# Optimization experiments

Hardware: AMD Instinct MI355X
Metric: run time of the kernel (lower is better)

The kernel has to match this reference:

```python
import jax, jax.numpy as jnp
import numpy as np

V, C, H, L, FC, OUT, WS = 512, 256, 4, 6, 1024, 192, 4
HD = C // H
B, T = 8, 1024


def setup_inputs() -> dict:
    key = jax.random.key(0)
    ks = jax.random.split(key, 24)
    d = {}
    d['emb'] = jax.random.normal(ks[0], (V, C), jnp.float32) * C ** -0.5
    d['Wq'] = jax.random.normal(ks[1], (L, C, C), jnp.float32) * 0.02
    d['Wk'] = jax.random.normal(ks[2], (L, C, C), jnp.float32) * 0.02
    d['Wv'] = jax.random.normal(ks[3], (L, C, C), jnp.float32) * 0.02
    d['Wo'] = jax.random.normal(ks[4], (L, C, C), jnp.float32) * 0.02
    d['bq'] = jnp.zeros((L, C), jnp.float32)
    d['bk'] = jnp.zeros((L, C), jnp.float32)
    d['bv'] = jnp.zeros((L, C), jnp.float32)
    d['bo'] = jnp.zeros((L, C), jnp.float32)
    d['rel_k'] = jax.random.normal(ks[5], (L, 2 * WS + 1, HD), jnp.float32) * HD ** -0.5
    d['rel_v'] = jax.random.normal(ks[6], (L, 2 * WS + 1, HD), jnp.float32) * HD ** -0.5
    d['ln1_g'] = jnp.ones((L, C), jnp.float32)
    d['ln1_b'] = jnp.zeros((L, C), jnp.float32)
    d['ln2_g'] = jnp.ones((L, C), jnp.float32)
    d['ln2_b'] = jnp.zeros((L, C), jnp.float32)
    d['ffn_w1'] = jax.random.normal(ks[7], (L, C, FC), jnp.float32) * 0.02
    d['ffn_b1'] = jnp.zeros((L, FC), jnp.float32)
    d['ffn_w2'] = jax.random.normal(ks[8], (L, FC, C), jnp.float32) * 0.02
    d['ffn_b2'] = jnp.zeros((L, C), jnp.float32)
    d['proj_w'] = jax.random.normal(ks[9], (2 * OUT, C), jnp.float32) * 0.02
    d['proj_b'] = jnp.zeros((2 * OUT,), jnp.float32)
    d['tokens'] = jax.random.randint(ks[10], (B, T), 0, V)
    d['x_lengths'] = jax.random.randint(ks[11], (B,), T // 2, T + 1)
    return d


def _rel_to_abs(x):
    # x: [B,H,L,2L-1] -> [B,H,L,L]
    b, h, l, _ = x.shape
    x = jnp.pad(x, ((0, 0), (0, 0), (0, 0), (0, 1)))
    x = x.reshape(b, h, l * 2 * l)
    x = jnp.pad(x, ((0, 0), (0, 0), (0, l - 1)))
    x = x.reshape(b, h, l + 1, 2 * l - 1)
    return x[:, :, :l, l - 1:]


def _abs_to_rel(x):
    # x: [B,H,L,L] -> [B,H,L,2L-1]
    b, h, l, _ = x.shape
    x = jnp.pad(x, ((0, 0), (0, 0), (0, 0), (0, l - 1)))
    x = x.reshape(b, h, l * (2 * l - 1))
    x = jnp.pad(x, ((0, 0), (0, 0), (l, 0)))
    x = x.reshape(b, h, l, 2 * l)
    return x[:, :, :, 1:]


def _layernorm(x, g, b):
    m = jnp.mean(x, -1, keepdims=True)
    v = jnp.var(x, -1, keepdims=True)
    return (x - m) * jax.lax.rsqrt(v + 1e-5) * g + b


def _pad_rel(emb, t):
    # [2*WS+1, HD] -> [2t-1, HD] (t > WS+1 here)
    p = t - (WS + 1)
    return jnp.pad(emb, ((p, p), (0, 0)))


def _forward(emb, Wq, Wk, Wv, Wo, bq, bk, bv, bo, rel_k, rel_v, ln1_g, ln1_b,
             ln2_g, ln2_b, ffn_w1, ffn_b1, ffn_w2, ffn_b2, proj_w, proj_b,
             tokens, x_lengths):
    b, t = tokens.shape
    x = emb[tokens] * jnp.sqrt(jnp.float32(C))          # [B,T,C]
    mask = (jnp.arange(t)[None, :] < x_lengths[:, None]).astype(x.dtype)  # [B,T]
    attn_mask = mask[:, None, None, :] * mask[:, None, :, None]           # [B,1,T,T]

    for i in range(L):
        q = (x @ Wq[i] + bq[i]).reshape(b, t, H, HD).transpose(0, 2, 1, 3)
        k = (x @ Wk[i] + bk[i]).reshape(b, t, H, HD).transpose(0, 2, 1, 3)
        v = (x @ Wv[i] + bv[i]).reshape(b, t, H, HD).transpose(0, 2, 1, 3)
        q = q * HD ** -0.5
        scores = jnp.einsum('bhqd,bhkd->bhqk', q, k)
        rk = _pad_rel(rel_k[i], t)                      # [2T-1,HD]
        scores = scores + _rel_to_abs(jnp.einsum('bhqd,md->bhqm', q, rk))
        scores = jnp.where(attn_mask > 0, scores, -1e4)
        p = jax.nn.softmax(scores, axis=-1)             # [B,H,T,T]
        o = jnp.einsum('bhqk,bhkd->bhqd', p, v)
        rv = _pad_rel(rel_v[i], t)
        o = o + jnp.einsum('bhqm,md->bhqd', _abs_to_rel(p), rv)
        o = o.transpose(0, 2, 1, 3).reshape(b, t, C) @ Wo[i] + bo[i]
        x = _layernorm(x + o, ln1_g[i], ln1_b[i])
        f = jax.nn.relu(x @ ffn_w1[i] + ffn_b1[i]) @ ffn_w2[i] + ffn_b2[i]
        x = _layernorm(x + f, ln2_g[i], ln2_b[i])
        x = x * mask[:, :, None]

    x_bct = x.transpose(0, 2, 1)                        # [B,C,T]
    stats = (jnp.einsum('oc,bct->bot', proj_w, x_bct) + proj_b[None, :, None])
    stats = stats * mask[:, None, :]
    m, logs = stats[:, :OUT], stats[:, OUT:]
    return x_bct, m, logs, mask[:, None, :]


def reference(emb, Wq, Wk, Wv, Wo, bq, bk, bv, bo, rel_k, rel_v, ln1_g, ln1_b,
              ln2_g, ln2_b, ffn_w1, ffn_b1, ffn_w2, ffn_b2, proj_w, proj_b,
              tokens, x_lengths):
    return _forward(emb, Wq, Wk, Wv, Wo, bq, bk, bv, bo, rel_k, rel_v, ln1_g,
                    ln1_b, ln2_g, ln2_b, ffn_w1, ffn_b1, ffn_w2, ffn_b2,
                    proj_w, proj_b, tokens, x_lengths)
```

## Files before the change

### kernel.cpp

```cpp
#include <hip/hip_runtime.h>

typedef unsigned short u16;
typedef __attribute__((ext_vector_type(8))) short bf16x8;
typedef __attribute__((ext_vector_type(4))) float f32x4;

#define CC   256
#define HH   4
#define HD   64
#define LL   6
#define FCD  1024
#define OUTD 192
#define WSZ  4
#define BB   8
#define TT   1024
#define BT   8192

#define OFF_XBCT 0
#define OFF_M    2097152
#define OFF_LOGS 3670016
#define OFF_MASK 5242880

#define WT_Q   0
#define WT_K   65536
#define WT_V   131072
#define WT_O   196608
#define WT_W1  262144
#define WT_W2  524288
#define WT_LAYER 786432
#define WT_TOTAL (6 * WT_LAYER)

__device__ __forceinline__ float bf2f(u16 u) {
  union { unsigned int i; float f; } v; v.i = ((unsigned int)u) << 16; return v.f;
}
__device__ __forceinline__ u16 f2bf(float f) {
  union { float f; unsigned int i; } v; v.f = f;
  unsigned int x = v.i;
  return (u16)((x + 0x7fffu + ((x >> 16) & 1u)) >> 16);
}
__device__ __forceinline__ void ldv4(const float* p, float* o) {
  float4 v = *reinterpret_cast<const float4*>(p);
  o[0] = v.x; o[1] = v.y; o[2] = v.z; o[3] = v.w;
}
__device__ __forceinline__ float ld_e(const float* p) { return *p; }
__device__ __forceinline__ float ld_e(const u16* p)   { return bf2f(*p); }
__device__ __forceinline__ void st_e(float* p, float v) { *p = v; }
__device__ __forceinline__ void st_e(u16* p, float v)   { *p = f2bf(v); }

__device__ __forceinline__ void gload16(const u16* g, u16* l) {
  __builtin_amdgcn_global_load_lds(
      (const __attribute__((address_space(1))) unsigned int*)g,
      (__attribute__((address_space(3))) unsigned int*)l, 16, 0, 0);
}

__device__ __forceinline__ void stage8(const float* p, u16* d) {
  float4 a = *reinterpret_cast<const float4*>(p);
  float4 b = *reinterpret_cast<const float4*>(p + 4);
  d[0] = f2bf(a.x); d[1] = f2bf(a.y); d[2] = f2bf(a.z); d[3] = f2bf(a.w);
  d[4] = f2bf(b.x); d[5] = f2bf(b.y); d[6] = f2bf(b.z); d[7] = f2bf(b.w);
}
__device__ __forceinline__ void stage8(const u16* p, u16* d) {
  ushort4 a = *reinterpret_cast<const ushort4*>(p);
  ushort4 b = *reinterpret_cast<const ushort4*>(p + 4);
  d[0] = a.x; d[1] = a.y; d[2] = a.z; d[3] = a.w;
  d[4] = b.x; d[5] = b.y; d[6] = b.z; d[7] = b.w;
}

__global__ __launch_bounds__(256) void tc_k(
    const float* __restrict__ W, u16* __restrict__ WT,
    int K, int N, int dstStride)
{
  __shared__ float tl[32][33];
  const int tid = threadIdx.x;
  const int lx = tid & 31;
  const int ly = tid >> 5;
  const int n0 = blockIdx.x << 5;
  const int k0 = blockIdx.y << 5;
  const int z  = blockIdx.z;
  const float* Ws = W + (size_t)z * K * N;
  u16* WTd = WT + (size_t)z * dstStride;
#pragma unroll
  for (int r = 0; r < 4; ++r)
    tl[ly + r * 8][lx] = Ws[(size_t)(k0 + ly + r * 8) * N + (n0 + lx)];
  __syncthreads();
#pragma unroll
  for (int r = 0; r < 4; ++r)
    WTd[(size_t)(n0 + ly + r * 8) * K + (k0 + lx)] = f2bf(tl[lx][ly + r * 8]);
}

__global__ __launch_bounds__(256) void embed_k(
    const float* __restrict__ emb, const int* __restrict__ tokens,
    float* __restrict__ X, u16* __restrict__ Xb)
{
  const int i = blockIdx.x * 256 + threadIdx.x;
  const int bt = i >> 6;
  const int c  = (i & 63) << 2;
  float4 e = *reinterpret_cast<const float4*>(emb + (size_t)tokens[bt] * CC + c);
  e.x *= 16.0f; e.y *= 16.0f; e.z *= 16.0f; e.w *= 16.0f;
  *reinterpret_cast<float4*>(X + (size_t)i * 4) = e;
  if (Xb)
    *reinterpret_cast<ushort4*>(Xb + (size_t)i * 4) =
        make_ushort4(f2bf(e.x), f2bf(e.y), f2bf(e.z), f2bf(e.w));
}

template <typename CT>
__global__ __launch_bounds__(256) void gemm_t_k(
    const u16* __restrict__ A, int lda, const u16* __restrict__ B, int ldb,
    const float* __restrict__ bias, CT* __restrict__ C, int ldc,
    int K, float ps, int relu, int accum)
{
  __shared__ __align__(16) u16 As[64 * 64];
  __shared__ __align__(16) u16 Bs[64 * 64];
  const int tid  = threadIdx.x;
  const int lane = tid & 63;
  const int wv   = tid >> 6;
  const int bm = blockIdx.y * 64;
  const int bn = blockIdx.x * 64;
  const int l15 = lane & 15;
  const int lq  = lane >> 4;
  const int sb0 = wv << 10;
  const int sb1 = sb0 + 512;
  const int r0  = (wv << 4) + (lane >> 3);
  const int r1  = r0 + 8;
  const int sc  = ((lane & 7) ^ (lane >> 3)) << 3;
  const int asw = (l15 & 7) << 3;

  f32x4 acc[4];
#pragma unroll
  for (int nt = 0; nt < 4; ++nt) acc[nt] = (f32x4){0.0f, 0.0f, 0.0f, 0.0f};

  for (int k0 = 0; k0 < K; k0 += 64) {
    gload16(A + (size_t)(bm + r0) * lda + (k0 + sc), As + sb0);
    gload16(A + (size_t)(bm + r1) * lda + (k0 + sc), As + sb1);
    gload16(B + (size_t)(bn + r0) * ldb + (k0 + sc), Bs + sb0);
    gload16(B + (size_t)(bn + r1) * ldb + (k0 + sc), Bs + sb1);
    __syncthreads();
#pragma unroll
    for (int s = 0; s < 2; ++s) {
      const int cbase = (s << 5) | (lq << 3);
      const bf16x8 af = *reinterpret_cast<const bf16x8*>(
          As + (((wv << 4) + l15) << 6) + (cbase ^ asw));
#pragma unroll
      for (int nt = 0; nt < 4; ++nt) {
        const bf16x8 bf = *reinterpret_cast<const bf16x8*>(
            Bs + (((nt << 4) + l15) << 6) + (cbase ^ asw));
        acc[nt] = __builtin_amdgcn_mfma_f32_16x16x32_bf16(af, bf, acc[nt], 0, 0, 0);
      }
    }
    __syncthreads();
  }

#pragma unroll
  for (int nt = 0; nt < 4; ++nt) {
#pragma unroll
    for (int r = 0; r < 4; ++r) {
      const int row = bm + (wv << 4) + (lq << 2) + r;
      const int col = bn + (nt << 4) + l15;
      float vv = acc[nt][r];
      if (bias) vv += bias[col];
      vv *= ps;
      if (relu) vv = fmaxf(vv, 0.0f);
      const size_t ci = (size_t)row * ldc + col;
      if (accum) vv += ld_e(C + ci);
      st_e(C + ci, vv);
    }
  }
}

__global__ __launch_bounds__(256) void gemm_qkv_k(
    const u16* __restrict__ Xb, const u16* __restrict__ WTl,
    const float* __restrict__ bq, const float* __restrict__ bk,
    const float* __restrict__ bv,
    u16* __restrict__ Qb, u16* __restrict__ Kb, u16* __restrict__ Vb)
{
  __shared__ __align__(16) u16 pool[2 * 64 * 64];
  u16* As = pool;
  u16* Bs = pool + 4096;
  const int tid  = threadIdx.x;
  const int lane = tid & 63;
  const int wv   = tid >> 6;
  const int bx = blockIdx.x;
  const int bm = blockIdx.y * 64;
  const int mi = bx >> 2;
  const int bnl = (bx & 3) << 6;
  const int bng = bx << 6;
  const int l15 = lane & 15;
  const int lq  = lane >> 4;
  const int sb0 = wv << 10;
  const int sb1 = sb0 + 512;
  const int r0  = (wv << 4) + (lane >> 3);
  const int r1  = r0 + 8;
  const int sc  = ((lane & 7) ^ (lane >> 3)) << 3;
  const int asw = (l15 & 7) << 3;

  const float* bias = (mi == 0) ? bq : (mi == 1) ? bk : bv;
  const float ps = (mi == 0) ? 0.125f : 1.0f;

  f32x4 acc[4];
#pragma unroll
  for (int nt = 0; nt < 4; ++nt) acc[nt] = (f32x4){0.0f, 0.0f, 0.0f, 0.0f};

  for (int k0 = 0; k0 < CC; k0 += 64) {
    gload16(Xb  + (size_t)(bm + r0) * CC + (k0 + sc), As + sb0);
    gload16(Xb  + (size_t)(bm + r1) * CC + (k0 + sc), As + sb1);
    gload16(WTl + (size_t)(bng + r0) * CC + (k0 + sc), Bs + sb0);
    gload16(WTl + (size_t)(bng + r1) * CC + (k0 + sc), Bs + sb1);
    __syncthreads();
#pragma unroll
    for (int s = 0; s < 2; ++s) {
      const int cbase = (s << 5) | (lq << 3);
      const bf16x8 af = *reinterpret_cast<const bf16x8*>(
          As + (((wv << 4) + l15) << 6) + (cbase ^ asw));
#pragma unroll
      for (int nt = 0; nt < 4; ++nt) {
        const bf16x8 bf = *reinterpret_cast<const bf16x8*>(
            Bs + (((nt << 4) + l15) << 6) + (cbase ^ asw));
        acc[nt] = __builtin_amdgcn_mfma_f32_16x16x32_bf16(af, bf, acc[nt], 0, 0, 0);
      }
    }
    __syncthreads();
  }

  if (mi != 2) {
    u16* Cp = (mi == 0) ? Qb : Kb;
#pragma unroll
    for (int nt = 0; nt < 4; ++nt) {
#pragma unroll
      for (int r = 0; r < 4; ++r) {
        const int row = bm + (wv << 4) + (lq << 2) + r;
        const int col = bnl + (nt << 4) + l15;
        Cp[(size_t)row * CC + col] = f2bf((acc[nt][r] + bias[col]) * ps);
      }
    }
  } else {
    u16* Ts = pool;
#pragma unroll
    for (int nt = 0; nt < 4; ++nt) {
#pragma unroll
      for (int r = 0; r < 4; ++r) {
        const int tl = (wv << 4) + (lq << 2) + r;
        const int dl = (nt << 4) + l15;
        Ts[dl * 72 + tl] = f2bf(acc[nt][r] + bias[bnl + dl]);
      }
    }
    __syncthreads();
    const int dl = tid >> 2;
    const size_t rowbase =
        ((size_t)((bm >> 10) * 256 + bnl + dl) << 10) + (bm & (TT - 1));
#pragma unroll
    for (int j = 0; j < 4; ++j) {
      const int c4 = ((tid & 3) << 2) + (j << 4);
      *reinterpret_cast<ushort4*>(Vb + rowbase + c4) =
          *reinterpret_cast<const ushort4*>(Ts + dl * 72 + c4);
    }
  }
}

__global__ __launch_bounds__(256) void gemm_ln_k(
    const u16* __restrict__ A, int lda, const u16* __restrict__ B, int ldb,
    const float* __restrict__ bias,
    float* __restrict__ X, u16* __restrict__ Xb,
    const float* __restrict__ g, const float* __restrict__ be,
    const int* __restrict__ xlen, int am, int K)
{
  __shared__ __align__(16) u16 As[16 * 64];
  __shared__ __align__(16) u16 Bs[256 * 64];
  __shared__ float part[16][4];
  __shared__ float part2[16][4];
  const int tid  = threadIdx.x;
  const int lane = tid & 63;
  const int wv   = tid >> 6;
  const int bm   = blockIdx.x << 4;
  const int l15  = lane & 15;
  const int lq   = lane >> 4;
  const int sc   = ((lane & 7) ^ (lane >> 3)) << 3;
  const int asw  = (l15 & 7) << 3;

  f32x4 acc[4];
#pragma unroll
  for (int nt = 0; nt < 4; ++nt) acc[nt] = (f32x4){0.0f, 0.0f, 0.0f, 0.0f};

  for (int k0 = 0; k0 < K; k0 += 64) {
    if (wv < 2)
      gload16(A + (size_t)(bm + (wv << 3) + (lane >> 3)) * lda + (k0 + sc),
              As + (wv << 9));
#pragma unroll
    for (int j = 0; j < 8; ++j)
      gload16(B + (size_t)((wv << 6) + (j << 3) + (lane >> 3)) * ldb + (k0 + sc),
              Bs + (wv << 12) + (j << 9));
    __syncthreads();
#pragma unroll
    for (int s = 0; s < 2; ++s) {
      const int cbase = (s << 5) | (lq << 3);
      const bf16x8 af = *reinterpret_cast<const bf16x8*>(
          As + (l15 << 6) + (cbase ^ asw));
#pragma unroll
      for (int nt = 0; nt < 4; ++nt) {
        const bf16x8 bf = *reinterpret_cast<const bf16x8*>(
            Bs + (((wv << 6) + (nt << 4) + l15) << 6) + (cbase ^ asw));
        acc[nt] = __builtin_amdgcn_mfma_f32_16x16x32_bf16(af, bf, acc[nt], 0, 0, 0);
      }
    }
    __syncthreads();
  }

  float v[4][4];
#pragma unroll
  for (int nt = 0; nt < 4; ++nt) {
    const int col = (wv << 6) + (nt << 4) + l15;
#pragma unroll
    for (int reg = 0; reg < 4; ++reg) {
      const int gr = bm + (lq << 2) + reg;
      v[nt][reg] = acc[nt][reg] + bias[col] + X[(size_t)gr * CC + col];
    }
  }
  float sr[4];
#pragma unroll
  for (int reg = 0; reg < 4; ++reg) {
    float s = v[0][reg] + v[1][reg] + v[2][reg] + v[3][reg];
    s += __shfl_xor(s, 1); s += __shfl_xor(s, 2);
    s += __shfl_xor(s, 4); s += __shfl_xor(s, 8);
    sr[reg] = s;
  }
  if (l15 == 0) {
#pragma unroll
    for (int reg = 0; reg < 4; ++reg) part[(lq << 2) + reg][wv] = sr[reg];
  }
  __syncthreads();
  float mean[4];
#pragma unroll
  for (int reg = 0; reg < 4; ++reg) {
    const int r = (lq << 2) + reg;
    mean[reg] = (part[r][0] + part[r][1] + part[r][2] + part[r][3]) * (1.0f / CC);
  }
#pragma unroll
  for (int reg = 0; reg < 4; ++reg) {
    float s2 = 0.0f;
#pragma unroll
    for (int nt = 0; nt < 4; ++nt) {
      v[nt][reg] -= mean[reg];
      s2 += v[nt][reg] * v[nt][reg];
    }
    s2 += __shfl_xor(s2, 1); s2 += __shfl_xor(s2, 2);
    s2 += __shfl_xor(s2, 4); s2 += __shfl_xor(s2, 8);
    sr[reg] = s2;
  }
  if (l15 == 0) {
#pragma unroll
    for (int reg = 0; reg < 4; ++reg) part2[(lq << 2) + reg][wv] = sr[reg];
  }
  __syncthreads();
#pragma unroll
  for (int reg = 0; reg < 4; ++reg) {
    const int r = (lq << 2) + reg;
    const int gr = bm + r;
    const int b = gr >> 10;
    const int t = gr & (TT - 1);
    const float var = (part2[r][0] + part2[r][1] + part2[r][2] + part2[r][3]) * (1.0f / CC);
    const float rs = rsqrtf(var + 1e-5f);
    const bool zero = (am && t >= xlen[b]);
#pragma unroll
    for (int nt = 0; nt < 4; ++nt) {
      const int col = (wv << 6) + (nt << 4) + l15;
      float y = v[nt][reg] * rs * g[col] + be[col];
      if (zero) y = 0.0f;
      X[(size_t)gr * CC + col] = y;
      Xb[(size_t)gr * CC + col] = f2bf(y);
    }
  }
}

template <typename AT, typename CT>
__global__ __launch_bounds__(256) void gemm_m_k(
    const AT* __restrict__ A, const float* __restrict__ W, int ldb,
    const float* __restrict__ bias, CT* __restrict__ C, int ldc,
    int K, float ps, int relu, int accum, int vtrans)
{
  __shared__ u16 As[64][40];
  __shared__ u16 Bs[64][40];
  const int tid  = threadIdx.x;
  const int lane = tid & 63;
  const int wv   = tid >> 6;
  const int bm = blockIdx.y * 64;
  const int bn = blockIdx.x * 64;
  const int l15 = lane & 15;
  const int lq  = lane >> 4;
  const int ar = tid >> 2;
  const int ak = (tid & 3) << 3;
  const int kr = tid & 31;
  const int nb = (tid >> 5) << 3;

  f32x4 acc[4];
#pragma unroll
  for (int nt = 0; nt < 4; ++nt) acc[nt] = (f32x4){0.0f, 0.0f, 0.0f, 0.0f};

  for (int k0 = 0; k0 < K; k0 += 32) {
    u16 t8[8];
    stage8(A + (size_t)(bm + ar) * K + (k0 + ak), t8);
    *reinterpret_cast<ushort4*>(&As[ar][ak]) =
        make_ushort4(t8[0], t8[1], t8[2], t8[3]);
    *reinterpret_cast<ushort4*>(&As[ar][ak + 4]) =
        make_ushort4(t8[4], t8[5], t8[6], t8[7]);
    float w8[8];
    ldv4(W + (size_t)(k0 + kr) * ldb + (bn + nb), w8);
    ldv4(W + (size_t)(k0 + kr) * ldb + (bn + nb + 4), w8 + 4);
#pragma unroll
    for (int j = 0; j < 8; ++j) Bs[nb + j][kr] = f2bf(w8[j]);
    __syncthreads();

    const bf16x8 af = *reinterpret_cast<const bf16x8*>(&As[(wv << 4) + l15][lq << 3]);
#pragma unroll
    for (int nt = 0; nt < 4; ++nt) {
      const bf16x8 bf = *reinterpret_cast<const bf16x8*>(&Bs[(nt << 4) + l15][lq << 3]);
      acc[nt] = __builtin_amdgcn_mfma_f32_16x16x32_bf16(af, bf, acc[nt], 0, 0, 0);
    }
    __syncthreads();
  }

#pragma unroll
  for (int nt = 0; nt < 4; ++nt) {
#pragma unroll
    for (int r = 0; r < 4; ++r) {
      const int row = bm + (wv << 4) + (lq << 2) + r;
      const int col = bn + (nt << 4) + l15;
      float vv = acc[nt][r];
      if (bias) vv += bias[col];
      vv *= ps;
      if (relu) vv = fmaxf(vv, 0.0f);
      if (vtrans) {
        const size_t dst = ((size_t)((row >> 10) * 256 + col) << 10) + (row & (TT - 1));
        st_e(C + dst, vv);
      } else {
        const size_t ci = (size_t)row * ldc + col;
        if (accum) vv += ld_e(C + ci);
        st_e(C + ci, vv);
      }
    }
  }
}

#define KLp(g) (KVpool + (g) * 4096)
#define VTp(g) (KVpool + 8192 + (g) * 4096)
__global__ __launch_bounds__(512, 4) void fattn_k(
    const u16* __restrict__ Qb, const u16* __restrict__ Kb,
    const u16* __restrict__ VbT, const float* __restrict__ rk,
    const float* __restrict__ rv, const int* __restrict__ xlen,
    u16* __restrict__ Ob)
{
  __shared__ __align__(16) u16 KVpool[4 * 64 * 64];
  __shared__ u16  Pl[2][64][64];
  __shared__ float rkl[9][64];
  __shared__ float rvl[9][68];
  __shared__ float qrel[64][12];
  __shared__ float bs_s[64][12];
  __shared__ float mrow_s[64];

  const int qt = blockIdx.x;
  const int bh = blockIdx.y;
  const int b  = bh >> 2;
  const int h  = bh & 3;
  const int tid  = threadIdx.x;
  const int lane = tid & 63;
  const int wv   = tid >> 6;
  const int grp  = wv >> 2;
  const int wvl  = wv & 3;
  const int gtid = tid & 255;
  const int l15  = lane & 15;
  const int lq   = lane >> 4;
  const int len = xlen[b];
  const int q0  = qt << 6;
  const int m0  = wvl << 4;

  if (q0 >= len) {
    for (int i = tid; i < 64 * 16; i += 512) {
      const int r = i >> 4, c4 = (i & 15) << 2;
      *reinterpret_cast<ushort4*>(
          Ob + (size_t)((b << 10) + q0 + r) * CC + (h << 6) + c4) =
          make_ushort4(0, 0, 0, 0);
    }
    return;
  }

  for (int i = tid; i < 9 * 64; i += 512) {
    rkl[i >> 6][i & 63] = rk[i];
    rvl[i >> 6][i & 63] = rv[i];
  }
  for (int i = tid; i < 64 * 16; i += 512) {
    const int r = i >> 4, c4 = (i & 15) << 2;
    *reinterpret_cast<ushort4*>(&Pl[0][r][c4]) = *reinterpret_cast<const ushort4*>(
        Qb + (size_t)((b << 10) + q0 + r) * CC + (h << 6) + c4);
  }
  for (int i = tid; i < 64 * 12; i += 512) (&bs_s[0][0])[i] = -3.0e38f;
  __syncthreads();
  for (int i = tid; i < 64 * 9; i += 512) {
    const int r = i / 9, j = i - r * 9;
    float s = 0.0f;
#pragma unroll 16
    for (int d = 0; d < 64; ++d) s += bf2f(Pl[0][r][d]) * rkl[j][d];
    qrel[r][j] = s;
  }
  __syncthreads();

  const bf16x8 qa0 = *reinterpret_cast<const bf16x8*>(&Pl[0][m0 + l15][lq << 3]);
  const bf16x8 qa1 = *reinterpret_cast<const bf16x8*>(&Pl[0][m0 + l15][32 + (lq << 3)]);

  f32x4 oacc[4];
#pragma unroll
  for (int nt = 0; nt < 4; ++nt) oacc[nt] = (f32x4){0.0f, 0.0f, 0.0f, 0.0f};
  float m_r[4] = {-3.0e38f, -3.0e38f, -3.0e38f, -3.0e38f};
  float l_r[4] = {0.0f, 0.0f, 0.0f, 0.0f};

  const int gr = gtid >> 2;
  const int gc = (gtid & 3) << 4;
  const int rswG = (gr & 7) << 3;
  const int c0w = gc ^ rswG;
  const int c1w = (gc + 8) ^ rswG;
  const int rswF = (l15 & 7) << 3;

  const int nkt = (len + 63) >> 6;
  const int nt0 = (nkt + 1) >> 1;
  const int myBeg = grp ? nt0 : 0;
  const int myEnd = grp ? nkt : nt0;

  u16* klp = KLp(grp);
  u16* vtp = VTp(grp);
  u16* plp = &Pl[grp][0][0];

  bf16x8 kp0, kp1, vq0, vq1;
  if (myBeg < myEnd) {
    const int k0 = myBeg << 6;
    const u16* p = Kb + (size_t)((b << 10) + k0 + gr) * CC + (h << 6) + gc;
    kp0 = *reinterpret_cast<const bf16x8*>(p);
    kp1 = *reinterpret_cast<const bf16x8*>(p + 8);
    const u16* pv = VbT + (size_t)((bh << 6) + gr) * TT + k0 + gc;
    vq0 = *reinterpret_cast<const bf16x8*>(pv);
    vq1 = *reinterpret_cast<const bf16x8*>(pv + 8);
  }

  for (int it = 0; it < nt0; ++it) {
    const int kt = myBeg + it;
    const bool act = (kt < myEnd);
    if (act) {
      *reinterpret_cast<bf16x8*>(klp + gr * 64 + c0w) = kp0;
      *reinterpret_cast<bf16x8*>(klp + gr * 64 + c1w) = kp1;
      *reinterpret_cast<bf16x8*>(vtp + gr * 64 + c0w) = vq0;
      *reinterpret_cast<bf16x8*>(vtp + gr * 64 + c1w) = vq1;
    }
    __syncthreads();

    if (act && kt + 1 < myEnd) {
      const int kn = (kt + 1) << 6;
      const u16* p = Kb + (size_t)((b << 10) + kn + gr) * CC + (h << 6) + gc;
      kp0 = *reinterpret_cast<const bf16x8*>(p);
      kp1 = *reinterpret_cast<const bf16x8*>(p + 8);
      const u16* pv = VbT + (size_t)((bh << 6) + gr) * TT + kn + gc;
      vq0 = *reinterpret_cast<const bf16x8*>(pv);
      vq1 = *reinterpret_cast<const bf16x8*>(pv + 8);
    }

    if (act) {
      const int k0 = kt << 6;
      f32x4 sacc[4];
#pragma unroll
      for (int nt = 0; nt < 4; ++nt) sacc[nt] = (f32x4){0.0f, 0.0f, 0.0f, 0.0f};
      __builtin_amdgcn_s_setprio(1);
#pragma unroll
      for (int nt = 0; nt < 4; ++nt) {
        const int row = (nt << 4) + l15;
        const bf16x8 b0 = *reinterpret_cast<const bf16x8*>(klp + row * 64 + ((lq << 3) ^ rswF));
        const bf16x8 b1 = *reinterpret_cast<const bf16x8*>(klp + row * 64 + ((32 + (lq << 3)) ^ rswF));
        sacc[nt] = __builtin_amdgcn_mfma_f32_16x16x32_bf16(qa0, b0, sacc[nt], 0, 0, 0);
        sacc[nt] = __builtin_amdgcn_mfma_f32_16x16x32_bf16(qa1, b1, sacc[nt], 0, 0, 0);
      }
      __builtin_amdgcn_s_setprio(0);
#pragma unroll
      for (int nt = 0; nt < 4; ++nt) {
#pragma unroll
        for (int reg = 0; reg < 4; ++reg) {
          const int m = m0 + (lq << 2) + reg;
          const int q = q0 + m;
          const int k = k0 + (nt << 4) + l15;
          float s = sacc[nt][reg];
          const int r = k - q;
          const bool band = (r >= -WSZ && r <= WSZ);
          if (band) s += qrel[m][r + WSZ];
          if (q >= len || k >= len) s = -10000.0f;
          if (band) bs_s[m][r + WSZ] = s;
          sacc[nt][reg] = s;
        }
      }
      float aa[4];
#pragma unroll
      for (int reg = 0; reg < 4; ++reg) {
        float mx = fmaxf(fmaxf(sacc[0][reg], sacc[1][reg]),
                         fmaxf(sacc[2][reg], sacc[3][reg]));
        mx = fmaxf(mx, __shfl_xor(mx, 1));
        mx = fmaxf(mx, __shfl_xor(mx, 2));
        mx = fmaxf(mx, __shfl_xor(mx, 4));
        mx = fmaxf(mx, __shfl_xor(mx, 8));
        const float mo = m_r[reg];
        const float mn = fmaxf(mo, mx);
        const float a = __expf(mo - mn);
        m_r[reg] = mn; aa[reg] = a; l_r[reg] *= a;
      }
#pragma unroll
      for (int reg = 0; reg < 4; ++reg) {
        const int m = m0 + (lq << 2) + reg;
        const int msw = (m & 7) << 3;
        const float mn = m_r[reg];
        float ssum = 0.0f;
#pragma unroll
        for (int nt = 0; nt < 4; ++nt) {
          const float p = __expf(sacc[nt][reg] - mn);
          ssum += p;
          plp[m * 64 + (((nt << 4) + l15) ^ msw)] = f2bf(p);
        }
        ssum += __shfl_xor(ssum, 1);
        ssum += __shfl_xor(ssum, 2);
        ssum += __shfl_xor(ssum, 4);
        ssum += __shfl_xor(ssum, 8);
        l_r[reg] += ssum;
      }
#pragma unroll
      for (int nt = 0; nt < 4; ++nt) {
#pragma unroll
        for (int reg = 0; reg < 4; ++reg) oacc[nt][reg] *= aa[reg];
      }
      {
        const int prow = m0 + l15;
        const bf16x8 p0 = *reinterpret_cast<const bf16x8*>(plp + prow * 64 + ((lq << 3) ^ rswF));
        const bf16x8 p1 = *reinterpret_cast<const bf16x8*>(plp + prow * 64 + ((32 + (lq << 3)) ^ rswF));
        __builtin_amdgcn_s_setprio(1);
#pragma unroll
        for (int nt = 0; nt < 4; ++nt) {
          const int row = (nt << 4) + l15;
          const bf16x8 v0 = *reinterpret_cast<const bf16x8*>(vtp + row * 64 + ((lq << 3) ^ rswF));
          const bf16x8 v1 = *reinterpret_cast<const bf16x8*>(vtp + row * 64 + ((32 + (lq << 3)) ^ rswF));
          oacc[nt] = __builtin_amdgcn_mfma_f32_16x16x32_bf16(p0, v0, oacc[nt], 0, 0, 0);
          oacc[nt] = __builtin_amdgcn_mfma_f32_16x16x32_bf16(p1, v1, oacc[nt], 0, 0, 0);
        }
        __builtin_amdgcn_s_setprio(0);
      }
    }
    __syncthreads();
  }

  float* Oc = (float*)KVpool;
  float* mxp = Oc + 64 * 68;
  float* lxp = mxp + 64;
  if (grp == 1) {
#pragma unroll
    for (int nt = 0; nt < 4; ++nt)
#pragma unroll
      for (int reg = 0; reg < 4; ++reg)
        Oc[(m0 + (lq << 2) + reg) * 68 + (nt << 4) + l15] = oacc[nt][reg];
    if (l15 == 0) {
#pragma unroll
      for (int reg = 0; reg < 4; ++reg) {
        mxp[m0 + (lq << 2) + reg] = m_r[reg];
        lxp[m0 + (lq << 2) + reg] = l_r[reg];
      }
    }
  }
  __syncthreads();
  if (grp == 0) {
    float a0c[4], a1c[4];
#pragma unroll
    for (int reg = 0; reg < 4; ++reg) {
      const int m = m0 + (lq << 2) + reg;
      const float m1 = mxp[m], l1 = lxp[m];
      const float mo = m_r[reg];
      const float mn = fmaxf(mo, m1);
      const float a0 = __expf(mo - mn);
      const float a1 = __expf(m1 - mn);
      m_r[reg] = mn;
      l_r[reg] = a0 * l_r[reg] + a1 * l1;
      a0c[reg] = a0; a1c[reg] = a1;
    }
#pragma unroll
    for (int nt = 0; nt < 4; ++nt)
#pragma unroll
      for (int reg = 0; reg < 4; ++reg) {
        const int m = m0 + (lq << 2) + reg;
        oacc[nt][reg] = a0c[reg] * oacc[nt][reg]
                      + a1c[reg] * Oc[m * 68 + (nt << 4) + l15];
      }
    if (l15 == 0) {
#pragma unroll
      for (int reg = 0; reg < 4; ++reg)
        mrow_s[m0 + (lq << 2) + reg] = m_r[reg];
    }
  }
  __syncthreads();
  for (int i = tid; i < 64 * 9; i += 512) {
    const int r = i / 9, j = i - r * 9;
    qrel[r][j] = __expf(bs_s[r][j] - mrow_s[r]);
  }
  __syncthreads();
  if (grp == 0) {
#pragma unroll
    for (int nt = 0; nt < 4; ++nt) {
#pragma unroll
      for (int reg = 0; reg < 4; ++reg) {
        const int m = m0 + (lq << 2) + reg;
        float o = oacc[nt][reg];
#pragma unroll
        for (int j = 0; j < 9; ++j) o += qrel[m][j] * rvl[j][(nt << 4) + l15];
        o *= 1.0f / l_r[reg];
        Ob[(size_t)((b << 10) + q0 + m) * CC + (h << 6) + (nt << 4) + l15] = f2bf(o);
      }
    }
  }
}

__global__ __launch_bounds__(256) void addln_k(
    float* __restrict__ X, u16* __restrict__ Xb, const float* __restrict__ R,
    const float* __restrict__ g, const float* __restrict__ be,
    const int* __restrict__ xlen, int am)
{
  const int tid = threadIdx.x;
  const int row = blockIdx.x * 4 + (tid >> 6);
  const int lane = tid & 63;
  const int b = row >> 10;
  const int t = row & (TT - 1);
  const size_t base = (size_t)row * CC + lane * 4;
  float4 xv = *reinterpret_cast<const float4*>(X + base);
  float4 rv = *reinterpret_cast<const float4*>(R + base);
  float v0 = xv.x + rv.x, v1 = xv.y + rv.y, v2 = xv.z + rv.z, v3 = xv.w + rv.w;
  float s = v0 + v1 + v2 + v3;
#pragma unroll
  for (int off = 32; off > 0; off >>= 1) s += __shfl_xor(s, off);
  const float mean = s * (1.0f / CC);
  const float d0 = v0 - mean, d1 = v1 - mean, d2 = v2 - mean, d3 = v3 - mean;
  float s2 = d0 * d0 + d1 * d1 + d2 * d2 + d3 * d3;
#pragma unroll
  for (int off = 32; off > 0; off >>= 1) s2 += __shfl_xor(s2, off);
  const float rs = rsqrtf(s2 * (1.0f / CC) + 1e-5f);
  const float4 gv = *reinterpret_cast<const float4*>(g + lane * 4);
  const float4 bv = *reinterpret_cast<const float4*>(be + lane * 4);
  float y0 = d0 * rs * gv.x + bv.x;
  float y1 = d1 * rs * gv.y + bv.y;
  float y2 = d2 * rs * gv.z + bv.z;
  float y3 = d3 * rs * gv.w + bv.w;
  if (am && t >= xlen[b]) { y0 = 0.0f; y1 = 0.0f; y2 = 0.0f; y3 = 0.0f; }
  *reinterpret_cast<float4*>(X + base) = make_float4(y0, y1, y2, y3);
  if (Xb)
    *reinterpret_cast<ushort4*>(Xb + base) =
        make_ushort4(f2bf(y0), f2bf(y1), f2bf(y2), f2bf(y3));
}

__global__ __launch_bounds__(256) void proj_k(
    const float* __restrict__ A, const float* __restrict__ W,
    const float* __restrict__ bias, const int* __restrict__ xlen,
    float* __restrict__ out)
{
  __shared__ u16 As[64][40];
  __shared__ u16 Bs[64][40];
  const int tid  = threadIdx.x;
  const int lane = tid & 63;
  const int wv   = tid >> 6;
  const int bm = blockIdx.y * 64;
  const int bn = blockIdx.x * 64;
  const int l15 = lane & 15;
  const int lq  = lane >> 4;
  const int ar = tid >> 2;
  const int ak = (tid & 3) << 3;

  f32x4 acc[4];
#pragma unroll
  for (int nt = 0; nt < 4; ++nt) acc[nt] = (f32x4){0.0f, 0.0f, 0.0f, 0.0f};

  for (int k0 = 0; k0 < CC; k0 += 32) {
    u16 t8[8];
    stage8(A + (size_t)(bm + ar) * CC + (k0 + ak), t8);
    *reinterpret_cast<ushort4*>(&As[ar][ak]) =
        make_ushort4(t8[0], t8[1], t8[2], t8[3]);
    *reinterpret_cast<ushort4*>(&As[ar][ak + 4]) =
        make_ushort4(t8[4], t8[5], t8[6], t8[7]);
    stage8(W + (size_t)(bn + ar) * CC + (k0 + ak), t8);
    *reinterpret_cast<ushort4*>(&Bs[ar][ak]) =
        make_ushort4(t8[0], t8[1], t8[2], t8[3]);
    *reinterpret_cast<ushort4*>(&Bs[ar][ak + 4]) =
        make_ushort4(t8[4], t8[5], t8[6], t8[7]);
    __syncthreads();

    const bf16x8 af = *reinterpret_cast<const bf16x8*>(&As[(wv << 4) + l15][lq << 3]);
#pragma unroll
    for (int nt = 0; nt < 4; ++nt) {
      const bf16x8 bf = *reinterpret_cast<const bf16x8*>(&Bs[(nt << 4) + l15][lq << 3]);
      acc[nt] = __builtin_amdgcn_mfma_f32_16x16x32_bf16(af, bf, acc[nt], 0, 0, 0);
    }
    __syncthreads();
  }

#pragma unroll
  for (int nt = 0; nt < 4; ++nt) {
#pragma unroll
    for (int r = 0; r < 4; ++r) {
      const int row = bm + (wv << 4) + (lq << 2) + r;
      const int bb = row >> 10;
      const int t  = row & (TT - 1);
      const int len = xlen[bb];
      const int o = bn + (nt << 4) + l15;
      float vv = acc[nt][r] + bias[o];
      if (t >= len) vv = 0.0f;
      const size_t dst = (o < OUTD)
          ? (size_t)OFF_M    + ((size_t)bb * OUTD + o) * TT + t
          : (size_t)OFF_LOGS + ((size_t)bb * OUTD + (o - OUTD)) * TT + t;
      out[dst] = vv;
    }
  }
}

__global__ __launch_bounds__(256) void pack_xbct_k(
    const float* __restrict__ X, float* __restrict__ out)
{
  __shared__ float tl[32][33];
  const int tid = threadIdx.x;
  const int lx = tid & 31;
  const int ly = tid >> 5;
  const int c0 = blockIdx.x << 5;
  const int t0 = blockIdx.y << 5;
  const int b  = blockIdx.z;
#pragma unroll
  for (int r = 0; r < 4; ++r)
    tl[ly + r * 8][lx] = X[(((size_t)(b << 10) + t0 + ly + r * 8) << 8) + c0 + lx];
  __syncthreads();
#pragma unroll
  for (int r = 0; r < 4; ++r)
    out[OFF_XBCT + (((size_t)b * 256 + c0 + ly + r * 8) << 10) + t0 + lx] =
        tl[lx][ly + r * 8];
}

__global__ __launch_bounds__(256) void pack_mask_k(
    const int* __restrict__ xlen, float* __restrict__ out)
{
  const int i = blockIdx.x * 256 + threadIdx.x;
  const int b = i >> 10;
  const int t = i & (TT - 1);
  out[OFF_MASK + i] = (t < xlen[b]) ? 1.0f : 0.0f;
}

extern "C" void kernel_launch(void* const* d_in, const int* in_sizes, int n_in,
                              void* d_out, int out_size, void* d_ws, size_t ws_size,
                              hipStream_t stream)
{
  (void)in_sizes; (void)n_in; (void)out_size;
  const float* emb   = (const float*)d_in[0];
  const float* Wq    = (const float*)d_in[1];
  const float* Wk    = (const float*)d_in[2];
  const float* Wv    = (const float*)d_in[3];
  const float* Wo    = (const float*)d_in[4];
  const float* bq    = (const float*)d_in[5];
  const float* bk    = (const float*)d_in[6];
  const float* bv    = (const float*)d_in[7];
  const float* bo    = (const float*)d_in[8];
  const float* relk  = (const float*)d_in[9];
  const float* relv  = (const float*)d_in[10];
  const float* ln1g  = (const float*)d_in[11];
  const float* ln1b  = (const float*)d_in[12];
  const float* ln2g  = (const float*)d_in[13];
  const float* ln2b  = (const float*)d_in[14];
  const float* W1    = (const float*)d_in[15];
  const float* b1    = (const float*)d_in[16];
  const float* W2    = (const float*)d_in[17];
  const float* b2    = (const float*)d_in[18];
  const float* projw = (const float*)d_in[19];
  const float* projb = (const float*)d_in[20];
  const int*   tokens = (const int*)d_in[21];
  const int*   xlen   = (const int*)d_in[22];
  float* out = (float*)d_out;

  const size_t TIER_B_WS = 26214400ull;
  const size_t TIER_A_WS = 38797312ull;
  const int tier = (ws_size >= TIER_A_WS) ? 0 : (ws_size >= TIER_B_WS) ? 1 : 2;

  float* X  = (float*)d_ws;
  u16* ObU = (u16*)(out + OFF_XBCT);
  u16* Kb  = (u16*)(out + OFF_M);
  u16* Vb  = (u16*)(out + OFF_LOGS);
  float* T5 = out + OFF_M;

  if (tier <= 1) {
    u16* Xb  = (u16*)(X + (size_t)BT * CC);
    u16* Wbf = Xb + (size_t)BT * CC;
    u16* pool = Wbf + WT_TOTAL;
    u16* Qb = pool;
    u16* Hc = pool;
    const int CH = (tier == 0) ? 1 : 4;
    const int Wn = FCD / CH;

    tc_k<<<dim3(8, 8, 6), 256, 0, stream>>>(Wq, Wbf + WT_Q, CC, CC, WT_LAYER);
    tc_k<<<dim3(8, 8, 6), 256, 0, stream>>>(Wk, Wbf + WT_K, CC, CC, WT_LAYER);
    tc_k<<<dim3(8, 8, 6), 256, 0, stream>>>(Wv, Wbf + WT_V, CC, CC, WT_LAYER);
    tc_k<<<dim3(8, 8, 6), 256, 0, stream>>>(Wo, Wbf + WT_O, CC, CC, WT_LAYER);
    tc_k<<<dim3(32, 8, 6), 256, 0, stream>>>(W1, Wbf + WT_W1, CC, FCD, WT_LAYER);
    tc_k<<<dim3(8, 32, 6), 256, 0, stream>>>(W2, Wbf + WT_W2, FCD, CC, WT_LAYER);

    embed_k<<<(BT * CC / 4) / 256, 256, 0, stream>>>(emb, tokens, X, Xb);

    const dim3 gQKV(12, BT / 64);
    const dim3 gA(16, BB * HH);
    const dim3 gP((2 * OUTD) / 64, BT / 64);

    for (int l = 0; l < LL; ++l) {
      const u16* WTl = Wbf + (size_t)l * WT_LAYER;
      gemm_qkv_k<<<gQKV, 256, 0, stream>>>(Xb, WTl, bq + (size_t)l * CC,
                                           bk + (size_t)l * CC, bv + (size_t)l * CC,
                                           Qb, Kb, Vb);
      fattn_k<<<gA, 512, 0, stream>>>(Qb, Kb, Vb,
                                      relk + (size_t)l * (2 * WSZ + 1) * HD,
                                      relv + (size_t)l * (2 * WSZ + 1) * HD, xlen, ObU);
      gemm_ln_k<<<BT / 16, 256, 0, stream>>>(ObU, CC, WTl + WT_O, CC,
                                             bo + (size_t)l * CC, X, Xb,
                                             ln1g + (size_t)l * CC,
                                             ln1b + (size_t)l * CC, xlen, 0, CC);
      if (CH == 1) {
        gemm_t_k<u16><<<dim3(FCD / 64, BT / 64), 256, 0, stream>>>(
            Xb, CC, WTl + WT_W1, CC, b1 + (size_t)l * FCD, Hc, FCD, CC,
            1.0f, 1, 0);
        gemm_ln_k<<<BT / 16, 256, 0, stream>>>(Hc, FCD, WTl + WT_W2, FCD,
                                               b2 + (size_t)l * CC, X, Xb,
                                               ln2g + (size_t)l * CC,
                                               ln2b + (size_t)l * CC, xlen, 1, FCD);
      } else {
        const dim3 gC(CC / 64, BT / 64);
        for (int c = 0; c < CH; ++c) {
          gemm_t_k<u16><<<dim3(Wn / 64, BT / 64), 256, 0, stream>>>(
              Xb, CC, WTl + WT_W1 + (size_t)c * Wn * CC, CC,
              b1 + (size_t)l * FCD + c * Wn, Hc, Wn, CC, 1.0f, 1, 0);
          gemm_t_k<float><<<gC, 256, 0, stream>>>(
              Hc, Wn, WTl + WT_W2 + (size_t)c * Wn, FCD,
              (c == 0) ? (b2 + (size_t)l * CC) : nullptr, T5, CC, Wn,
              1.0f, 0, (c > 0));
        }
        addln_k<<<BT / 4, 256, 0, stream>>>(X, Xb, T5, ln2g + (size_t)l * CC,
                                            ln2b + (size_t)l * CC, xlen, 1);
      }
    }

    proj_k<<<gP, 256, 0, stream>>>(X, projw, projb, xlen, out);
  } else {
    u16* pool = (u16*)(X + (size_t)BT * CC);
    u16* Qb = pool;
    u16* Hc = pool;

    embed_k<<<(BT * CC / 4) / 256, 256, 0, stream>>>(emb, tokens, X, nullptr);

    const dim3 gC(CC / 64, BT / 64);
    const dim3 gA(16, BB * HH);
    const dim3 gP((2 * OUTD) / 64, BT / 64);

    for (int l = 0; l < LL; ++l) {
      const float* Wq_l = Wq + (size_t)l * CC * CC;
      const float* Wk_l = Wk + (size_t)l * CC * CC;
      const float* Wv_l = Wv + (size_t)l * CC * CC;
      const float* Wo_l = Wo + (size_t)l * CC * CC;

      gemm_m_k<float, u16><<<gC, 256, 0, stream>>>(X, Wq_l, CC, bq + (size_t)l * CC,
                                                   Qb, CC, CC, 0.125f, 0, 0, 0);
      gemm_m_k<float, u16><<<gC, 256, 0, stream>>>(X, Wk_l, CC, bk + (size_t)l * CC,
                                                   Kb, CC, CC, 1.0f, 0, 0, 0);
      gemm_m_k<float, u16><<<gC, 256, 0, stream>>>(X, Wv_l, CC, bv + (size_t)l * CC,
                                                   Vb, CC, CC, 1.0f, 0, 0, 1);
      fattn_k<<<gA, 512, 0, stream>>>(Qb, Kb, Vb,
                                      relk + (size_t)l * (2 * WSZ + 1) * HD,
                                      relv + (size_t)l * (2 * WSZ + 1) * HD, xlen, ObU);
      gemm_m_k<u16, float><<<gC, 256, 0, stream>>>(ObU, Wo_l, CC, bo + (size_t)l * CC,
                                                   T5, CC, CC, 1.0f, 0, 0, 0);
      addln_k<<<BT / 4, 256, 0, stream>>>(X, nullptr, T5, ln1g + (size_t)l * CC,
                                          ln1b + (size_t)l * CC, xlen, 0);
      for (int c = 0; c < 4; ++c) {
        gemm_m_k<float, u16><<<gC, 256, 0, stream>>>(X, W1 + (size_t)l * CC * FCD + c * 256,
                                                     FCD, b1 + (size_t)l * FCD + c * 256,
                                                     Hc, 256, CC, 1.0f, 1, 0, 0);
        gemm_m_k<u16, float><<<gC, 256, 0, stream>>>(Hc,
                                                     W2 + (size_t)l * FCD * CC + (size_t)c * 256 * CC,
                                                     CC, (c == 0) ? (b2 + (size_t)l * CC) : nullptr,
                                                     T5, CC, 256, 1.0f, 0, (c > 0), 0);
      }
      addln_k<<<BT / 4, 256, 0, stream>>>(X, nullptr, T5, ln2g + (size_t)l * CC,
                                          ln2b + (size_t)l * CC, xlen, 1);
    }

    proj_k<<<gP, 256, 0, stream>>>(X, projw, projb, xlen, out);
  }

  pack_xbct_k<<<dim3(CC / 32, TT / 32, BB), 256, 0, stream>>>(X, out);
  pack_mask_k<<<(BB * TT) / 256, 256, 0, stream>>>(xlen, out);
}
```

Measured before the change: 691.6 us.

## Read K/V fragments straight from global memory in fused attention, dropping LDS staging

The attention kernel no longer stages each 64-key K and V^T tile through shared memory with register prefetch and block-wide barriers. Each wave now loads its MFMA B-operand fragments directly from global memory, relying on L1/L2 to serve the reads that waves in a group repeat. This frees the 32KB KV pool, and the partial-output merge now reuses the P and rel_k shared buffers. The aim is higher occupancy and no per-iteration __syncthreads, at the cost of exposed global-load latency with no software prefetch and redundant cache traffic.

```diff
diff --git a/kernel.cpp b/kernel.cpp
--- a/kernel.cpp
+++ b/kernel.cpp
@@ -438,16 +438,13 @@
   }
 }
 
-#define KLp(g) (KVpool + (g) * 4096)
-#define VTp(g) (KVpool + 8192 + (g) * 4096)
 __global__ __launch_bounds__(512, 4) void fattn_k(
     const u16* __restrict__ Qb, const u16* __restrict__ Kb,
     const u16* __restrict__ VbT, const float* __restrict__ rk,
     const float* __restrict__ rv, const int* __restrict__ xlen,
     u16* __restrict__ Ob)
 {
-  __shared__ __align__(16) u16 KVpool[4 * 64 * 64];
-  __shared__ u16  Pl[2][64][64];
+  __shared__ __align__(16) u16 Pl[2][64][64];
   __shared__ float rkl[9][64];
   __shared__ float rvl[9][68];
   __shared__ float qrel[64][12];
@@ -463,7 +460,6 @@
   const int wv   = tid >> 6;
   const int grp  = wv >> 2;
   const int wvl  = wv & 3;
-  const int gtid = tid & 255;
   const int l15  = lane & 15;
   const int lq   = lane >> 4;
   const int len = xlen[b];
@@ -502,6 +498,7 @@
 
   const bf16x8 qa0 = *reinterpret_cast<const bf16x8*>(&Pl[0][m0 + l15][lq << 3]);
   const bf16x8 qa1 = *reinterpret_cast<const bf16x8*>(&Pl[0][m0 + l15][32 + (lq << 3)]);
+  __syncthreads();
 
   f32x4 oacc[4];
 #pragma unroll
@@ -509,11 +506,6 @@
   float m_r[4] = {-3.0e38f, -3.0e38f, -3.0e38f, -3.0e38f};
   float l_r[4] = {0.0f, 0.0f, 0.0f, 0.0f};
 
-  const int gr = gtid >> 2;
-  const int gc = (gtid & 3) << 4;
-  const int rswG = (gr & 7) << 3;
-  const int c0w = gc ^ rswG;
-  const int c1w = (gc + 8) ^ rswG;
   const int rswF = (l15 & 7) << 3;
 
   const int nkt = (len + 63) >> 6;
@@ -521,138 +513,107 @@
   const int myBeg = grp ? nt0 : 0;
   const int myEnd = grp ? nkt : nt0;
 
-  u16* klp = KLp(grp);
-  u16* vtp = VTp(grp);
   u16* plp = &Pl[grp][0][0];
-
-  bf16x8 kp0, kp1, vq0, vq1;
-  if (myBeg < myEnd) {
-    const int k0 = myBeg << 6;
-    const u16* p = Kb + (size_t)((b << 10) + k0 + gr) * CC + (h << 6) + gc;
-    kp0 = *reinterpret_cast<const bf16x8*>(p);
-    kp1 = *reinterpret_cast<const bf16x8*>(p + 8);
-    const u16* pv = VbT + (size_t)((bh << 6) + gr) * TT + k0 + gc;
-    vq0 = *reinterpret_cast<const bf16x8*>(pv);
-    vq1 = *reinterpret_cast<const bf16x8*>(pv + 8);
-  }
-
-  for (int it = 0; it < nt0; ++it) {
-    const int kt = myBeg + it;
-    const bool act = (kt < myEnd);
-    if (act) {
-      *reinterpret_cast<bf16x8*>(klp + gr * 64 + c0w) = kp0;
-      *reinterpret_cast<bf16x8*>(klp + gr * 64 + c1w) = kp1;
-      *reinterpret_cast<bf16x8*>(vtp + gr * 64 + c0w) = vq0;
-      *reinterpret_cast<bf16x8*>(vtp + gr * 64 + c1w) = vq1;
-    }
-    __syncthreads();
-
-    if (act && kt + 1 < myEnd) {
-      const int kn = (kt + 1) << 6;
-      const u16* p = Kb + (size_t)((b << 10) + kn + gr) * CC + (h << 6) + gc;
-      kp0 = *reinterpret_cast<const bf16x8*>(p);
-      kp1 = *reinterpret_cast<const bf16x8*>(p + 8);
-      const u16* pv = VbT + (size_t)((bh << 6) + gr) * TT + kn + gc;
-      vq0 = *reinterpret_cast<const bf16x8*>(pv);
-      vq1 = *reinterpret_cast<const bf16x8*>(pv + 8);
-    }
-
-    if (act) {
-      const int k0 = kt << 6;
-      f32x4 sacc[4];
-#pragma unroll
-      for (int nt = 0; nt < 4; ++nt) sacc[nt] = (f32x4){0.0f, 0.0f, 0.0f, 0.0f};
+  const u16* kbase = Kb + (size_t)((b << 10)) * CC + (h << 6);
+  const u16* vbase = VbT + ((size_t)(bh << 6)) * TT;
+
+  for (int kt = myBeg; kt < myEnd; ++kt) {
+    const int k0 = kt << 6;
+    f32x4 sacc[4];
+#pragma unroll
+    for (int nt = 0; nt < 4; ++nt) sacc[nt] = (f32x4){0.0f, 0.0f, 0.0f, 0.0f};
+    __builtin_amdgcn_s_setprio(1);
+#pragma unroll
+    for (int nt = 0; nt < 4; ++nt) {
+      const int row = (nt << 4) + l15;
+      const u16* kp = kbase + (size_t)(k0 + row) * CC + (lq << 3);
+      const bf16x8 b0 = *reinterpret_cast<const bf16x8*>(kp);
+      const bf16x8 b1 = *reinterpret_cast<const bf16x8*>(kp + 32);
+      sacc[nt] = __builtin_amdgcn_mfma_f32_16x16x32_bf16(qa0, b0, sacc[nt], 0, 0, 0);
+      sacc[nt] = __builtin_amdgcn_mfma_f32_16x16x32_bf16(qa1, b1, sacc[nt], 0, 0, 0);
+    }
+    __builtin_amdgcn_s_setprio(0);
+#pragma unroll
+    for (int nt = 0; nt < 4; ++nt) {
+#pragma unroll
+      for (int reg = 0; reg < 4; ++reg) {
+        const int m = m0 + (lq << 2) + reg;
+        const int q = q0 + m;
+        const int k = k0 + (nt << 4) + l15;
+        float s = sacc[nt][reg];
+        const int r = k - q;
+        const bool band = (r >= -WSZ && r <= WSZ);
+        if (band) s += qrel[m][r + WSZ];
+        if (q >= len || k >= len) s = -10000.0f;
+        if (band) bs_s[m][r + WSZ] = s;
+        sacc[nt][reg] = s;
+      }
+    }
+    float aa[4];
+#pragma unroll
+    for (int reg = 0; reg < 4; ++reg) {
+      float mx = fmaxf(fmaxf(sacc[0][reg], sacc[1][reg]),
+                       fmaxf(sacc[2][reg], sacc[3][reg]));
+      mx = fmaxf(mx, __shfl_xor(mx, 1));
+      mx = fmaxf(mx, __shfl_xor(mx, 2));
+      mx = fmaxf(mx, __shfl_xor(mx, 4));
+      mx = fmaxf(mx, __shfl_xor(mx, 8));
+      const float mo = m_r[reg];
+      const float mn = fmaxf(mo, mx);
+      const float a = __expf(mo - mn);
+      m_r[reg] = mn; aa[reg] = a; l_r[reg] *= a;
+    }
+#pragma unroll
+    for (int reg = 0; reg < 4; ++reg) {
+      const int m = m0 + (lq << 2) + reg;
+      const int msw = (m & 7) << 3;
+      const float mn = m_r[reg];
+      float ssum = 0.0f;
+#pragma unroll
+      for (int nt = 0; nt < 4; ++nt) {
+        const float p = __expf(sacc[nt][reg] - mn);
+        ssum += p;
+        plp[m * 64 + (((nt << 4) + l15) ^ msw)] = f2bf(p);
+      }
+      ssum += __shfl_xor(ssum, 1);
+      ssum += __shfl_xor(ssum, 2);
+      ssum += __shfl_xor(ssum, 4);
+      ssum += __shfl_xor(ssum, 8);
+      l_r[reg] += ssum;
+    }
+#pragma unroll
+    for (int nt = 0; nt < 4; ++nt) {
+#pragma unroll
+      for (int reg = 0; reg < 4; ++reg) oacc[nt][reg] *= aa[reg];
+    }
+    {
+      const int prow = m0 + l15;
+      const bf16x8 p0 = *reinterpret_cast<const bf16x8*>(plp + prow * 64 + ((lq << 3) ^ rswF));
+      const bf16x8 p1 = *reinterpret_cast<const bf16x8*>(plp + prow * 64 + ((32 + (lq << 3)) ^ rswF));
       __builtin_amdgcn_s_setprio(1);
 #pragma unroll
       for (int nt = 0; nt < 4; ++nt) {
         const int row = (nt << 4) + l15;
-        const bf16x8 b0 = *reinterpret_cast<const bf16x8*>(klp + row * 64 + ((lq << 3) ^ rswF));
-        const bf16x8 b1 = *reinterpret_cast<const bf16x8*>(klp + row * 64 + ((32 + (lq << 3)) ^ rswF));
-        sacc[nt] = __builtin_amdgcn_mfma_f32_16x16x32_bf16(qa0, b0, sacc[nt], 0, 0, 0);
-        sacc[nt] = __builtin_amdgcn_mfma_f32_16x16x32_bf16(qa1, b1, sacc[nt], 0, 0, 0);
+        const u16* vp = vbase + (size_t)row * TT + k0 + (lq << 3);
+        const bf16x8 v0 = *reinterpret_cast<const bf16x8*>(vp);
+        const bf16x8 v1 = *reinterpret_cast<const bf16x8*>(vp + 32);
+        oacc[nt] = __builtin_amdgcn_mfma_f32_16x16x32_bf16(p0, v0, oacc[nt], 0, 0, 0);
+        oacc[nt] = __builtin_amdgcn_mfma_f32_16x16x32_bf16(p1, v1, oacc[nt], 0, 0, 0);
       }
       __builtin_amdgcn_s_setprio(0);
-#pragma unroll
-      for (int nt = 0; nt < 4; ++nt) {
-#pragma unroll
-        for (int reg = 0; reg < 4; ++reg) {
-          const int m = m0 + (lq << 2) + reg;
-          const int q = q0 + m;
-          const int k = k0 + (nt << 4) + l15;
-          float s = sacc[nt][reg];
-          const int r = k - q;
-          const bool band = (r >= -WSZ && r <= WSZ);
-          if (band) s += qrel[m][r + WSZ];
-          if (q >= len || k >= len) s = -10000.0f;
-          if (band) bs_s[m][r + WSZ] = s;
-          sacc[nt][reg] = s;
-        }
-      }
-      float aa[4];
-#pragma unroll
-      for (int reg = 0; reg < 4; ++reg) {
-        float mx = fmaxf(fmaxf(sacc[0][reg], sacc[1][reg]),
-                         fmaxf(sacc[2][reg], sacc[3][reg]));
-        mx = fmaxf(mx, __shfl_xor(mx, 1));
-        mx = fmaxf(mx, __shfl_xor(mx, 2));
-        mx = fmaxf(mx, __shfl_xor(mx, 4));
-        mx = fmaxf(mx, __shfl_xor(mx, 8));
-        const float mo = m_r[reg];
-        const float mn = fmaxf(mo, mx);
-        const float a = __expf(mo - mn);
-        m_r[reg] = mn; aa[reg] = a; l_r[reg] *= a;
-      }
-#pragma unroll
-      for (int reg = 0; reg < 4; ++reg) {
-        const int m = m0 + (lq << 2) + reg;
-        const int msw = (m & 7) << 3;
-        const float mn = m_r[reg];
-        float ssum = 0.0f;
-#pragma unroll
-        for (int nt = 0; nt < 4; ++nt) {
-          const float p = __expf(sacc[nt][reg] - mn);
-          ssum += p;
-          plp[m * 64 + (((nt << 4) + l15) ^ msw)] = f2bf(p);
-        }
-        ssum += __shfl_xor(ssum, 1);
-        ssum += __shfl_xor(ssum, 2);
-        ssum += __shfl_xor(ssum, 4);
-        ssum += __shfl_xor(ssum, 8);
-        l_r[reg] += ssum;
-      }
-#pragma unroll
-      for (int nt = 0; nt < 4; ++nt) {
-#pragma unroll
-        for (int reg = 0; reg < 4; ++reg) oacc[nt][reg] *= aa[reg];
-      }
-      {
-        const int prow = m0 + l15;
-        const bf16x8 p0 = *reinterpret_cast<const bf16x8*>(plp + prow * 64 + ((lq << 3) ^ rswF));
-        const bf16x8 p1 = *reinterpret_cast<const bf16x8*>(plp + prow * 64 + ((32 + (lq << 3)) ^ rswF));
-        __builtin_amdgcn_s_setprio(1);
-#pragma unroll
-        for (int nt = 0; nt < 4; ++nt) {
-          const int row = (nt << 4) + l15;
-          const bf16x8 v0 = *reinterpret_cast<const bf16x8*>(vtp + row * 64 + ((lq << 3) ^ rswF));
-          const bf16x8 v1 = *reinterpret_cast<const bf16x8*>(vtp + row * 64 + ((32 + (lq << 3)) ^ rswF));
-          oacc[nt] = __builtin_amdgcn_mfma_f32_16x16x32_bf16(p0, v0, oacc[nt], 0, 0, 0);
-          oacc[nt] = __builtin_amdgcn_mfma_f32_16x16x32_bf16(p1, v1, oacc[nt], 0, 0, 0);
-        }
-        __builtin_amdgcn_s_setprio(0);
-      }
-    }
-    __syncthreads();
-  }
-
-  float* Oc = (float*)KVpool;
-  float* mxp = Oc + 64 * 68;
+    }
+  }
+
+  __syncthreads();
+  float* Oc = (float*)&Pl[0][0][0];
+  float* mxp = (float*)&rkl[0][0];
   float* lxp = mxp + 64;
   if (grp == 1) {
 #pragma unroll
     for (int nt = 0; nt < 4; ++nt)
 #pragma unroll
       for (int reg = 0; reg < 4; ++reg)
-        Oc[(m0 + (lq << 2) + reg) * 68 + (nt << 4) + l15] = oacc[nt][reg];
+        Oc[(m0 + (lq << 2) + reg) * 64 + (nt << 4) + l15] = oacc[nt][reg];
     if (l15 == 0) {
 #pragma unroll
       for (int reg = 0; reg < 4; ++reg) {
@@ -682,7 +643,7 @@
       for (int reg = 0; reg < 4; ++reg) {
         const int m = m0 + (lq << 2) + reg;
         oacc[nt][reg] = a0c[reg] * oacc[nt][reg]
-                      + a1c[reg] * Oc[m * 68 + (nt << 4) + l15];
+                      + a1c[reg] * Oc[m * 64 + (nt << 4) + l15];
       }
     if (l15 == 0) {
 #pragma unroll
```

After: 862.6 us. +24.7%, slower.
